# Kernel tuning notes

Measured on AMD Instinct MI355X. Metric: run time of the kernel, lower is better.

## Reference

```python
import jax, jax.numpy as jnp
import numpy as np

H = 64  # LSTM units for both layers
T = 128  # sequence length
D = 128  # input feature dim
B = 2048  # batch

def setup_inputs() -> dict:
    key = jax.random.key(0)
    ks = jax.random.split(key, 7)
    s_in = 1.0 / np.sqrt(D)
    s_h = 1.0 / np.sqrt(H)
    return {
        "x": jax.random.normal(ks[0], (B, T, D), dtype=jnp.float32),
        # Keras LSTM weights: kernel [in, 4H], recurrent_kernel [H, 4H], bias [4H]
        # gate order: i, f, g (cell candidate), o
        "W1": jax.random.normal(ks[1], (D, 4 * H), dtype=jnp.float32) * s_in,
        "U1": jax.random.normal(ks[2], (H, 4 * H), dtype=jnp.float32) * s_h,
        "b1": jnp.zeros((4 * H,), dtype=jnp.float32),
        "W2": jax.random.normal(ks[3], (H, 4 * H), dtype=jnp.float32) * s_h,
        "U2": jax.random.normal(ks[4], (H, 4 * H), dtype=jnp.float32) * s_h,
        "b2": jnp.zeros((4 * H,), dtype=jnp.float32),
    }

def _lstm(x, W, U, b, act):
    """Keras-faithful LSTM, return_sequences=True, zero init state.
    x: [B, T, D_in] -> hs: [B, T, H]
    recurrent_activation = sigmoid; `act` is the cell/output activation.
    """
    Bsz = x.shape[0]
    # Precompute input projections for all timesteps (one big GEMM).
    xz = jnp.einsum('btd,dg->btg', x, W) + b  # [B, T, 4H]
    xz = jnp.swapaxes(xz, 0, 1)  # [T, B, 4H]

    def step(carry, zt):
        h, c = carry
        z = zt + h @ U  # [B, 4H]
        i, f, g, o = jnp.split(z, 4, axis=-1)
        i = jax.nn.sigmoid(i)
        f = jax.nn.sigmoid(f)
        g = act(g)
        o = jax.nn.sigmoid(o)
        c = f * c + i * g
        h = o * act(c)
        return (h, c), h

    init = (jnp.zeros((Bsz, H), x.dtype), jnp.zeros((Bsz, H), x.dtype))
    _, hs = jax.lax.scan(step, init, xz)  # hs: [T, B, H]
    return jnp.swapaxes(hs, 0, 1)  # [B, T, H]

def reference(x, W1, U1, b1, W2, U2, b2):
    h1 = _lstm(x, W1, U1, b1, jnp.tanh)           # layer 1: default tanh
    h2 = _lstm(h1, W2, U2, b2, jax.nn.sigmoid)    # layer 2: activation='sigmoid'
    return h2.reshape(h2.shape[0], T * H, 1)      # Reshape((8192, 1))
```

## Files before the change

### kernel.cpp

```cpp
#include <hip/hip_runtime.h>
#include <stdint.h>

typedef __attribute__((ext_vector_type(8))) short short8;
typedef __attribute__((ext_vector_type(4))) short short4_t;
typedef __attribute__((ext_vector_type(4))) float floatx4;

#define TT 128
#define DD 128

#define BARRIER_LDS() asm volatile("s_waitcnt lgkmcnt(0)\n\ts_barrier" ::: "memory")

__device__ __forceinline__ short f2bf(float f) {
  union { float f; uint32_t u; } v; v.f = f;
  uint32_t u = v.u;
  u += 0x7fffu + ((u >> 16) & 1u);
  return (short)(u >> 16);
}

__device__ __forceinline__ float sigf(float x) {
  return __builtin_amdgcn_rcpf(1.f + __expf(-x));
}
__device__ __forceinline__ float tanhf_(float x) {
  return 2.f * __builtin_amdgcn_rcpf(1.f + __expf(-2.f * x)) - 1.f;
}

__global__ void wtrans_all(const float* __restrict__ W1, const float* __restrict__ U1,
                           const float* __restrict__ W2, const float* __restrict__ U2,
                           short* __restrict__ w1t, short* __restrict__ u1t,
                           short* __restrict__ w2t, short* __restrict__ u2t) {
  int n = blockIdx.x;
  int k = threadIdx.x;
  w1t[n * 128 + k] = f2bf(W1[k * 256 + n]);
  if (k < 64) {
    u1t[n * 64 + k] = f2bf(U1[k * 256 + n]);
    w2t[n * 64 + k] = f2bf(W2[k * 256 + n]);
    u2t[n * 64 + k] = f2bf(U2[k * 256 + n]);
  }
}

__global__ __launch_bounds__(512, 2) void lstm_fused(
    const float* __restrict__ x,
    const short* __restrict__ w1t, const short* __restrict__ u1t,
    const short* __restrict__ w2t, const short* __restrict__ u2t,
    const float* __restrict__ b1, const float* __restrict__ b2,
    float* __restrict__ out) {
  __shared__ short hb1[2][8 * 80];
  __shared__ short hb2[2][8 * 80];
  __shared__ short xbuf[2][8 * 144];

  const int tid = threadIdx.x;
  const int w = tid >> 6;
  const bool isL1 = (w < 4);
  const int wg = w & 3;
  const int lane = tid & 63;
  const int mrow = lane & 15;
  const int quad = lane >> 4;
  const int rowbase = blockIdx.x * 8;
  const int colw = wg * 16 + mrow;
  const int br_a = 2 * (mrow >> 2) + (mrow & 1);

  short8 wA[4][4], uA[4][2];
  float bias[4];
  if (isL1) {
#pragma unroll
    for (int g = 0; g < 4; ++g) {
      const int n = g * 4 + wg;
#pragma unroll
      for (int s = 0; s < 4; ++s)
        wA[g][s] = *(const short8*)(w1t + n * 2048 + mrow * 128 + quad * 8 + s * 32);
#pragma unroll
      for (int s = 0; s < 2; ++s)
        uA[g][s] = *(const short8*)(u1t + n * 1024 + mrow * 64 + quad * 8 + s * 32);
      bias[g] = b1[g * 64 + colw];
    }
  } else {
#pragma unroll
    for (int g = 0; g < 4; ++g) {
      const int n = g * 4 + wg;
#pragma unroll
      for (int s = 0; s < 2; ++s) {
        wA[g][s]     = *(const short8*)(w2t + n * 1024 + mrow * 64 + quad * 8 + s * 32);
        wA[g][2 + s] = *(const short8*)(u2t + n * 1024 + mrow * 64 + quad * 8 + s * 32);
      }
      bias[g] = b2[g * 64 + colw];
    }
  }

  const int tid2 = tid & 255;
  const int sxr = tid2 >> 5;
  const int sxc = (tid2 & 31) * 4;
  const float* xload = x + (size_t)(rowbase + sxr) * (TT * DD) + sxc;

  short8 h1f[2], xh[4];
#pragma unroll
  for (int s = 0; s < 2; ++s)
#pragma unroll
    for (int j = 0; j < 8; ++j) h1f[s][j] = 0;
#pragma unroll
  for (int s = 0; s < 4; ++s)
#pragma unroll
    for (int j = 0; j < 8; ++j) xh[s][j] = 0;
  float cc[2] = {0.f, 0.f};
  floatx4 xnext;

  for (int idx = tid; idx < 2 * 8 * 80; idx += 512) ((short*)hb2)[idx] = 0;
  if (!isL1) {
    floatx4 x0 = *(const floatx4*)xload;
    short4_t v;
#pragma unroll
    for (int j = 0; j < 4; ++j) v[j] = f2bf(x0[j]);
    *(short4_t*)&xbuf[0][sxr * 144 + sxc] = v;
    xnext = *(const floatx4*)(xload + DD);
  }
  BARRIER_LDS();
  if (isL1) {
#pragma unroll
    for (int s = 0; s < 4; ++s)
      xh[s] = *(const short8*)&xbuf[0][br_a * 144 + (quad + 4 * s) * 8];
  }

  float* outp = out + (size_t)rowbase * 8192 + colw;

#pragma unroll 1
  for (int i = 0; i <= TT; ++i) {
    const int p = i & 1;

    if (isL1) {
      if (i < TT) {
        floatx4 acc[4];
#pragma unroll
        for (int g = 0; g < 4; ++g) acc[g] = floatx4{0.f, 0.f, 0.f, 0.f};
#pragma unroll
        for (int g = 0; g < 4; ++g) {
#pragma unroll
          for (int s = 0; s < 4; ++s)
            acc[g] = __builtin_amdgcn_mfma_f32_16x16x32_bf16(xh[s], wA[g][s], acc[g], 0, 0, 0);
#pragma unroll
          for (int s = 0; s < 2; ++s)
            acc[g] = __builtin_amdgcn_mfma_f32_16x16x32_bf16(h1f[s], uA[g][s], acc[g], 0, 0, 0);
        }
#pragma unroll
        for (int r = 0; r < 2; ++r) {
          float ig = sigf(acc[0][r] + bias[0]);
          float fg = sigf(acc[1][r] + bias[1]);
          float gg = tanhf_(acc[2][r] + bias[2]);
          float og = sigf(acc[3][r] + bias[3]);
          float c = fg * cc[r] + ig * gg;
          cc[r] = c;
          float h = og * tanhf_(c);
          hb1[p][(2 * quad + r) * 80 + colw] = f2bf(h);
        }
      }
    } else {
      {
        short4_t v;
#pragma unroll
        for (int j = 0; j < 4; ++j) v[j] = f2bf(xnext[j]);
        *(short4_t*)&xbuf[1 - p][sxr * 144 + sxc] = v;
        int tn = (i + 2 < TT) ? i + 2 : TT - 1;
        xnext = *(const floatx4*)(xload + (size_t)tn * DD);
      }
      if (i >= 1) {
        floatx4 acc[4];
#pragma unroll
        for (int g = 0; g < 4; ++g) acc[g] = floatx4{0.f, 0.f, 0.f, 0.f};
#pragma unroll
        for (int g = 0; g < 4; ++g) {
#pragma unroll
          for (int s = 0; s < 2; ++s)
            acc[g] = __builtin_amdgcn_mfma_f32_16x16x32_bf16(h1f[s], wA[g][s], acc[g], 0, 0, 0);
#pragma unroll
          for (int s = 0; s < 2; ++s)
            acc[g] = __builtin_amdgcn_mfma_f32_16x16x32_bf16(xh[s], wA[g][2 + s], acc[g], 0, 0, 0);
        }
#pragma unroll
        for (int r = 0; r < 2; ++r) {
          float ig = sigf(acc[0][r] + bias[0]);
          float fg = sigf(acc[1][r] + bias[1]);
          float gg = sigf(acc[2][r] + bias[2]);
          float og = sigf(acc[3][r] + bias[3]);
          float c = fg * cc[r] + ig * gg;
          cc[r] = c;
          float h = og * sigf(c);
          hb2[p][(2 * quad + r) * 80 + colw] = f2bf(h);
          outp[(size_t)(2 * quad + r) * 8192 + (i - 1) * 64] = h;
        }
      }
    }

    BARRIER_LDS();

    if (i < TT) {
      if (isL1) {
#pragma unroll
        for (int s = 0; s < 2; ++s)
          h1f[s] = *(const short8*)&hb1[p][br_a * 80 + (quad + 4 * s) * 8];
#pragma unroll
        for (int s = 0; s < 4; ++s)
          xh[s] = *(const short8*)&xbuf[1 - p][br_a * 144 + (quad + 4 * s) * 8];
      } else {
#pragma unroll
        for (int s = 0; s < 2; ++s) {
          h1f[s] = *(const short8*)&hb1[p][br_a * 80 + (quad + 4 * s) * 8];
          xh[s]  = *(const short8*)&hb2[p][br_a * 80 + (quad + 4 * s) * 8];
        }
      }
    }
  }
}

extern "C" void kernel_launch(void* const* d_in, const int* in_sizes, int n_in,
                              void* d_out, int out_size, void* d_ws, size_t ws_size,
                              hipStream_t stream) {
  const float* x  = (const float*)d_in[0];
  const float* W1 = (const float*)d_in[1];
  const float* U1 = (const float*)d_in[2];
  const float* b1 = (const float*)d_in[3];
  const float* W2 = (const float*)d_in[4];
  const float* U2 = (const float*)d_in[5];
  const float* b2 = (const float*)d_in[6];
  float* out = (float*)d_out;

  short* w1t = (short*)d_ws;
  short* u1t = w1t + 32768;
  short* w2t = u1t + 16384;
  short* u2t = w2t + 16384;

  hipLaunchKernelGGL(wtrans_all, dim3(256), dim3(128), 0, stream,
                     W1, U1, W2, U2, w1t, u1t, w2t, u2t);
  hipLaunchKernelGGL(lstm_fused, dim3(256), dim3(512), 0, stream,
                     x, w1t, u1t, w2t, u2t, b1, b2, out);
}
```

Measured before the change: 287.4 us.

## Split LSTM into four wave-group stages pipelining input and recurrent projections

The block grows from 512 to 1024 threads, organised as four 4-wave jobs. Job 0 computes the x·W1 projection, job 1 does the U1 recurrence, job 2 computes h1·W2 and job 3 does the U2 recurrence and writes the output. Partial gate sums pass between jobs through new double-buffered fp32 LDS arrays, skewed by one timestep per stage. This takes the non-recurrent GEMM work off the serial critical path of each layer, at the cost of more LDS, more barrier participants per step, three extra pipeline steps, and launch bounds of (1024,4) that may force tight register limits.

```diff
diff --git a/kernel.cpp b/kernel.cpp
--- a/kernel.cpp
+++ b/kernel.cpp
@@ -4,6 +4,7 @@
 typedef __attribute__((ext_vector_type(8))) short short8;
 typedef __attribute__((ext_vector_type(4))) short short4_t;
 typedef __attribute__((ext_vector_type(4))) float floatx4;
+typedef __attribute__((ext_vector_type(2))) float floatx2;
 
 #define TT 128
 #define DD 128
@@ -38,7 +39,7 @@
   }
 }
 
-__global__ __launch_bounds__(512, 2) void lstm_fused(
+__global__ __launch_bounds__(1024, 4) void lstm_fused(
     const float* __restrict__ x,
     const short* __restrict__ w1t, const short* __restrict__ u1t,
     const short* __restrict__ w2t, const short* __restrict__ u2t,
@@ -47,10 +48,12 @@
   __shared__ short hb1[2][8 * 80];
   __shared__ short hb2[2][8 * 80];
   __shared__ short xbuf[2][8 * 144];
+  __shared__ float zx[2][256][10];
+  __shared__ float zw2[2][256][10];
 
   const int tid = threadIdx.x;
   const int w = tid >> 6;
-  const bool isL1 = (w < 4);
+  const int job = w >> 2;
   const int wg = w & 3;
   const int lane = tid & 63;
   const int mrow = lane & 15;
@@ -59,85 +62,94 @@
   const int colw = wg * 16 + mrow;
   const int br_a = 2 * (mrow >> 2) + (mrow & 1);
 
-  short8 wA[4][4], uA[4][2];
-  float bias[4];
-  if (isL1) {
-#pragma unroll
-    for (int g = 0; g < 4; ++g) {
-      const int n = g * 4 + wg;
-#pragma unroll
-      for (int s = 0; s < 4; ++s)
-        wA[g][s] = *(const short8*)(w1t + n * 2048 + mrow * 128 + quad * 8 + s * 32);
-#pragma unroll
-      for (int s = 0; s < 2; ++s)
-        uA[g][s] = *(const short8*)(u1t + n * 1024 + mrow * 64 + quad * 8 + s * 32);
-      bias[g] = b1[g * 64 + colw];
-    }
-  } else {
-#pragma unroll
-    for (int g = 0; g < 4; ++g) {
-      const int n = g * 4 + wg;
-#pragma unroll
-      for (int s = 0; s < 2; ++s) {
-        wA[g][s]     = *(const short8*)(w2t + n * 1024 + mrow * 64 + quad * 8 + s * 32);
-        wA[g][2 + s] = *(const short8*)(u2t + n * 1024 + mrow * 64 + quad * 8 + s * 32);
-      }
-      bias[g] = b2[g * 64 + colw];
-    }
+  for (int idx = tid; idx < 2 * 8 * 80; idx += 1024) {
+    ((short*)hb1)[idx] = 0;
+    ((short*)hb2)[idx] = 0;
   }
 
   const int tid2 = tid & 255;
   const int sxr = tid2 >> 5;
   const int sxc = (tid2 & 31) * 4;
   const float* xload = x + (size_t)(rowbase + sxr) * (TT * DD) + sxc;
-
-  short8 h1f[2], xh[4];
-#pragma unroll
-  for (int s = 0; s < 2; ++s)
-#pragma unroll
-    for (int j = 0; j < 8; ++j) h1f[s][j] = 0;
-#pragma unroll
-  for (int s = 0; s < 4; ++s)
-#pragma unroll
-    for (int j = 0; j < 8; ++j) xh[s][j] = 0;
-  float cc[2] = {0.f, 0.f};
-  floatx4 xnext;
-
-  for (int idx = tid; idx < 2 * 8 * 80; idx += 512) ((short*)hb2)[idx] = 0;
-  if (!isL1) {
+  floatx4 xcur, xnxt;
+  if (job == 0) {
     floatx4 x0 = *(const floatx4*)xload;
     short4_t v;
 #pragma unroll
     for (int j = 0; j < 4; ++j) v[j] = f2bf(x0[j]);
     *(short4_t*)&xbuf[0][sxr * 144 + sxc] = v;
-    xnext = *(const floatx4*)(xload + DD);
-  }
+    xcur = *(const floatx4*)(xload + DD);
+    xnxt = *(const floatx4*)(xload + 2 * DD);
+  }
+
   BARRIER_LDS();
-  if (isL1) {
-#pragma unroll
-    for (int s = 0; s < 4; ++s)
-      xh[s] = *(const short8*)&xbuf[0][br_a * 144 + (quad + 4 * s) * 8];
-  }
-
-  float* outp = out + (size_t)rowbase * 8192 + colw;
-
-#pragma unroll 1
-  for (int i = 0; i <= TT; ++i) {
-    const int p = i & 1;
-
-    if (isL1) {
+
+  if (job == 0) {
+    short8 wA[4][4];
+#pragma unroll
+    for (int g = 0; g < 4; ++g) {
+      const int n = g * 4 + wg;
+#pragma unroll
+      for (int s = 0; s < 4; ++s)
+        wA[g][s] = *(const short8*)(w1t + n * 2048 + mrow * 128 + quad * 8 + s * 32);
+    }
+#pragma unroll 1
+    for (int i = 0; i <= TT + 2; ++i) {
+      const int p = i & 1;
       if (i < TT) {
         floatx4 acc[4];
 #pragma unroll
         for (int g = 0; g < 4; ++g) acc[g] = floatx4{0.f, 0.f, 0.f, 0.f};
 #pragma unroll
+        for (int s = 0; s < 4; ++s) {
+          short8 xh = *(const short8*)&xbuf[p][br_a * 144 + (quad + 4 * s) * 8];
+#pragma unroll
+          for (int g = 0; g < 4; ++g)
+            acc[g] = __builtin_amdgcn_mfma_f32_16x16x32_bf16(xh, wA[g][s], acc[g], 0, 0, 0);
+        }
+        if (i <= TT - 2) {
+          short4_t v;
+#pragma unroll
+          for (int j = 0; j < 4; ++j) v[j] = f2bf(xcur[j]);
+          *(short4_t*)&xbuf[1 - p][sxr * 144 + sxc] = v;
+          xcur = xnxt;
+          const int tn = (i + 3 < TT) ? (i + 3) : (TT - 1);
+          xnxt = *(const floatx4*)(xload + (size_t)tn * DD);
+        }
+#pragma unroll
+        for (int g = 0; g < 4; ++g)
+          *(floatx2*)&zx[p][g * 64 + colw][2 * quad] = floatx2{acc[g][0], acc[g][1]};
+      }
+      BARRIER_LDS();
+    }
+  } else if (job == 1) {
+    short8 uA[4][2];
+    float bias[4];
+#pragma unroll
+    for (int g = 0; g < 4; ++g) {
+      const int n = g * 4 + wg;
+#pragma unroll
+      for (int s = 0; s < 2; ++s)
+        uA[g][s] = *(const short8*)(u1t + n * 1024 + mrow * 64 + quad * 8 + s * 32);
+      bias[g] = b1[g * 64 + colw];
+    }
+    float cc[2] = {0.f, 0.f};
+#pragma unroll 1
+    for (int i = 0; i <= TT + 2; ++i) {
+      const int p = i & 1;
+      if (i >= 1 && i <= TT) {
+        floatx4 acc[4];
+#pragma unroll
         for (int g = 0; g < 4; ++g) {
-#pragma unroll
-          for (int s = 0; s < 4; ++s)
-            acc[g] = __builtin_amdgcn_mfma_f32_16x16x32_bf16(xh[s], wA[g][s], acc[g], 0, 0, 0);
-#pragma unroll
-          for (int s = 0; s < 2; ++s)
-            acc[g] = __builtin_amdgcn_mfma_f32_16x16x32_bf16(h1f[s], uA[g][s], acc[g], 0, 0, 0);
+          floatx2 z = *(const floatx2*)&zx[1 - p][g * 64 + colw][2 * quad];
+          acc[g] = floatx4{z[0], z[1], z[0], z[1]};
+        }
+#pragma unroll
+        for (int s = 0; s < 2; ++s) {
+          short8 hf = *(const short8*)&hb1[p][br_a * 80 + (quad + 4 * s) * 8];
+#pragma unroll
+          for (int g = 0; g < 4; ++g)
+            acc[g] = __builtin_amdgcn_mfma_f32_16x16x32_bf16(hf, uA[g][s], acc[g], 0, 0, 0);
         }
 #pragma unroll
         for (int r = 0; r < 2; ++r) {
@@ -148,30 +160,70 @@
           float c = fg * cc[r] + ig * gg;
           cc[r] = c;
           float h = og * tanhf_(c);
-          hb1[p][(2 * quad + r) * 80 + colw] = f2bf(h);
-        }
-      }
-    } else {
-      {
-        short4_t v;
-#pragma unroll
-        for (int j = 0; j < 4; ++j) v[j] = f2bf(xnext[j]);
-        *(short4_t*)&xbuf[1 - p][sxr * 144 + sxc] = v;
-        int tn = (i + 2 < TT) ? i + 2 : TT - 1;
-        xnext = *(const floatx4*)(xload + (size_t)tn * DD);
-      }
-      if (i >= 1) {
+          hb1[1 - p][(2 * quad + r) * 80 + colw] = f2bf(h);
+        }
+      }
+      BARRIER_LDS();
+    }
+  } else if (job == 2) {
+    short8 wB[4][2];
+#pragma unroll
+    for (int g = 0; g < 4; ++g) {
+      const int n = g * 4 + wg;
+#pragma unroll
+      for (int s = 0; s < 2; ++s)
+        wB[g][s] = *(const short8*)(w2t + n * 1024 + mrow * 64 + quad * 8 + s * 32);
+    }
+#pragma unroll 1
+    for (int i = 0; i <= TT + 2; ++i) {
+      const int p = i & 1;
+      if (i >= 2 && i <= TT + 1) {
         floatx4 acc[4];
 #pragma unroll
         for (int g = 0; g < 4; ++g) acc[g] = floatx4{0.f, 0.f, 0.f, 0.f};
 #pragma unroll
+        for (int s = 0; s < 2; ++s) {
+          short8 hf = *(const short8*)&hb1[p][br_a * 80 + (quad + 4 * s) * 8];
+#pragma unroll
+          for (int g = 0; g < 4; ++g)
+            acc[g] = __builtin_amdgcn_mfma_f32_16x16x32_bf16(hf, wB[g][s], acc[g], 0, 0, 0);
+        }
+#pragma unroll
+        for (int g = 0; g < 4; ++g)
+          *(floatx2*)&zw2[p][g * 64 + colw][2 * quad] = floatx2{acc[g][0], acc[g][1]};
+      }
+      BARRIER_LDS();
+    }
+  } else {
+    short8 uB[4][2];
+    float bias[4];
+#pragma unroll
+    for (int g = 0; g < 4; ++g) {
+      const int n = g * 4 + wg;
+#pragma unroll
+      for (int s = 0; s < 2; ++s)
+        uB[g][s] = *(const short8*)(u2t + n * 1024 + mrow * 64 + quad * 8 + s * 32);
+      bias[g] = b2[g * 64 + colw];
+    }
+    float cc[2] = {0.f, 0.f};
+    float* outp = out + (size_t)rowbase * 8192 + colw;
+#pragma unroll 1
+    for (int i = 0; i <= TT + 2; ++i) {
+      const int p = i & 1;
+      if (i >= 3) {
+        const int t = i - 3;
+        floatx4 acc[4];
+#pragma unroll
         for (int g = 0; g < 4; ++g) {
-#pragma unroll
-          for (int s = 0; s < 2; ++s)
-            acc[g] = __builtin_amdgcn_mfma_f32_16x16x32_bf16(h1f[s], wA[g][s], acc[g], 0, 0, 0);
-#pragma unroll
-          for (int s = 0; s < 2; ++s)
-            acc[g] = __builtin_amdgcn_mfma_f32_16x16x32_bf16(xh[s], wA[g][2 + s], acc[g], 0, 0, 0);
+          floatx2 z = *(const floatx2*)&zw2[1 - p][g * 64 + colw][2 * quad];
+          acc[g] = floatx4{z[0], z[1], z[0], z[1]};
+        }
+#pragma unroll
+        for (int s = 0; s < 2; ++s) {
+          short8 hf = *(const short8*)&hb2[p][br_a * 80 + (quad + 4 * s) * 8];
+#pragma unroll
+          for (int g = 0; g < 4; ++g)
+            acc[g] = __builtin_amdgcn_mfma_f32_16x16x32_bf16(hf, uB[g][s], acc[g], 0, 0, 0);
         }
 #pragma unroll
         for (int r = 0; r < 2; ++r) {
@@ -182,29 +234,11 @@
           float c = fg * cc[r] + ig * gg;
           cc[r] = c;
           float h = og * sigf(c);
-          hb2[p][(2 * quad + r) * 80 + colw] = f2bf(h);
-          outp[(size_t)(2 * quad + r) * 8192 + (i - 1) * 64] = h;
-        }
-      }
-    }
-
-    BARRIER_LDS();
-
-    if (i < TT) {
-      if (isL1) {
-#pragma unroll
-        for (int s = 0; s < 2; ++s)
-          h1f[s] = *(const short8*)&hb1[p][br_a * 80 + (quad + 4 * s) * 8];
-#pragma unroll
-        for (int s = 0; s < 4; ++s)
-          xh[s] = *(const short8*)&xbuf[1 - p][br_a * 144 + (quad + 4 * s) * 8];
-      } else {
-#pragma unroll
-        for (int s = 0; s < 2; ++s) {
-          h1f[s] = *(const short8*)&hb1[p][br_a * 80 + (quad + 4 * s) * 8];
-          xh[s]  = *(const short8*)&hb2[p][br_a * 80 + (quad + 4 * s) * 8];
-        }
-      }
+          hb2[1 - p][(2 * quad + r) * 80 + colw] = f2bf(h);
+          outp[(size_t)(2 * quad + r) * 8192 + t * 64] = h;
+        }
+      }
+      BARRIER_LDS();
     }
   }
 }
@@ -228,6 +262,6 @@
 
   hipLaunchKernelGGL(wtrans_all, dim3(256), dim3(128), 0, stream,
                      W1, U1, W2, U2, w1t, u1t, w2t, u2t);
-  hipLaunchKernelGGL(lstm_fused, dim3(256), dim3(512), 0, stream,
+  hipLaunchKernelGGL(lstm_fused, dim3(256), dim3(1024), 0, stream,
                      x, w1t, u1t, w2t, u2t, b1, b2, out);
 }
```

Measured after the change: 310.2 us. 7.9% more time.

## Halve batch rows per block to double grid size and raise occupancy

Applied to the files above, without the earlier changes.

Each block now handles 4 batch rows instead of 8, and the grid grows to 512 blocks. In the MFMA tiles the rows are duplicated, so each lane evaluates the gate nonlinearities for a single row instead of two. Launch bounds are raised to 4 blocks per CU, and the x prefetch goes two steps ahead. The aim is to spread the latency-bound sequential recurrence across more CUs and more resident waves, shortening the per-step critical path. The cost is that half of the MFMA work is redundant, and register pressure under the tighter launch bounds could cause spills.

```diff
diff --git a/kernel.cpp b/kernel.cpp
--- a/kernel.cpp
+++ b/kernel.cpp
@@ -2,8 +2,9 @@
 #include <stdint.h>
 
 typedef __attribute__((ext_vector_type(8))) short short8;
-typedef __attribute__((ext_vector_type(4))) short short4_t;
+typedef __attribute__((ext_vector_type(2))) short short2_t;
 typedef __attribute__((ext_vector_type(4))) float floatx4;
+typedef __attribute__((ext_vector_type(2))) float floatx2;
 
 #define TT 128
 #define DD 128
@@ -38,15 +39,15 @@
   }
 }
 
-__global__ __launch_bounds__(512, 2) void lstm_fused(
+__global__ __launch_bounds__(512, 4) void lstm_fused(
     const float* __restrict__ x,
     const short* __restrict__ w1t, const short* __restrict__ u1t,
     const short* __restrict__ w2t, const short* __restrict__ u2t,
     const float* __restrict__ b1, const float* __restrict__ b2,
     float* __restrict__ out) {
-  __shared__ short hb1[2][8 * 80];
-  __shared__ short hb2[2][8 * 80];
-  __shared__ short xbuf[2][8 * 144];
+  __shared__ short hb1[2][4 * 80];
+  __shared__ short hb2[2][4 * 80];
+  __shared__ short xbuf[2][4 * 144];
 
   const int tid = threadIdx.x;
   const int w = tid >> 6;
@@ -55,9 +56,11 @@
   const int lane = tid & 63;
   const int mrow = lane & 15;
   const int quad = lane >> 4;
-  const int rowbase = blockIdx.x * 8;
+  const int rowbase = blockIdx.x * 4;
   const int colw = wg * 16 + mrow;
-  const int br_a = 2 * (mrow >> 2) + (mrow & 1);
+  const int br_a = (2 * (mrow >> 2) + (mrow & 1)) & 3;
+  const bool rsel = (quad >> 1) & 1;
+  const int erow = (2 * quad + (quad >> 1)) & 3;
 
   short8 wA[4][4], uA[4][2];
   float bias[4];
@@ -87,8 +90,8 @@
   }
 
   const int tid2 = tid & 255;
-  const int sxr = tid2 >> 5;
-  const int sxc = (tid2 & 31) * 4;
+  const int sxr = tid2 >> 6;
+  const int sxc = (tid2 & 63) * 2;
   const float* xload = x + (size_t)(rowbase + sxr) * (TT * DD) + sxc;
 
   short8 h1f[2], xh[4];
@@ -100,17 +103,17 @@
   for (int s = 0; s < 4; ++s)
 #pragma unroll
     for (int j = 0; j < 8; ++j) xh[s][j] = 0;
-  float cc[2] = {0.f, 0.f};
-  floatx4 xnext;
-
-  for (int idx = tid; idx < 2 * 8 * 80; idx += 512) ((short*)hb2)[idx] = 0;
+  float cc = 0.f;
+  floatx2 xcur, xnxt;
+
+  for (int idx = tid; idx < 2 * 4 * 80; idx += 512) ((short*)hb2)[idx] = 0;
   if (!isL1) {
-    floatx4 x0 = *(const floatx4*)xload;
-    short4_t v;
-#pragma unroll
-    for (int j = 0; j < 4; ++j) v[j] = f2bf(x0[j]);
-    *(short4_t*)&xbuf[0][sxr * 144 + sxc] = v;
-    xnext = *(const floatx4*)(xload + DD);
+    floatx2 x0 = *(const floatx2*)xload;
+    short2_t v;
+    v[0] = f2bf(x0[0]); v[1] = f2bf(x0[1]);
+    *(short2_t*)&xbuf[0][sxr * 144 + sxc] = v;
+    xcur = *(const floatx2*)(xload + DD);
+    xnxt = *(const floatx2*)(xload + 2 * DD);
   }
   BARRIER_LDS();
   if (isL1) {
@@ -139,26 +142,28 @@
           for (int s = 0; s < 2; ++s)
             acc[g] = __builtin_amdgcn_mfma_f32_16x16x32_bf16(h1f[s], uA[g][s], acc[g], 0, 0, 0);
         }
-#pragma unroll
-        for (int r = 0; r < 2; ++r) {
-          float ig = sigf(acc[0][r] + bias[0]);
-          float fg = sigf(acc[1][r] + bias[1]);
-          float gg = tanhf_(acc[2][r] + bias[2]);
-          float og = sigf(acc[3][r] + bias[3]);
-          float c = fg * cc[r] + ig * gg;
-          cc[r] = c;
+        float za[4];
+#pragma unroll
+        for (int g = 0; g < 4; ++g) za[g] = rsel ? acc[g][1] : acc[g][0];
+        {
+          float ig = sigf(za[0] + bias[0]);
+          float fg = sigf(za[1] + bias[1]);
+          float gg = tanhf_(za[2] + bias[2]);
+          float og = sigf(za[3] + bias[3]);
+          float c = fg * cc + ig * gg;
+          cc = c;
           float h = og * tanhf_(c);
-          hb1[p][(2 * quad + r) * 80 + colw] = f2bf(h);
+          hb1[p][erow * 80 + colw] = f2bf(h);
         }
       }
     } else {
-      {
-        short4_t v;
-#pragma unroll
-        for (int j = 0; j < 4; ++j) v[j] = f2bf(xnext[j]);
-        *(short4_t*)&xbuf[1 - p][sxr * 144 + sxc] = v;
-        int tn = (i + 2 < TT) ? i + 2 : TT - 1;
-        xnext = *(const floatx4*)(xload + (size_t)tn * DD);
+      if (i <= TT - 2) {
+        short2_t v;
+        v[0] = f2bf(xcur[0]); v[1] = f2bf(xcur[1]);
+        *(short2_t*)&xbuf[1 - p][sxr * 144 + sxc] = v;
+        xcur = xnxt;
+        const int tn = (i + 3 < TT) ? (i + 3) : (TT - 1);
+        xnxt = *(const floatx2*)(xload + (size_t)tn * DD);
       }
       if (i >= 1) {
         floatx4 acc[4];
@@ -173,17 +178,19 @@
           for (int s = 0; s < 2; ++s)
             acc[g] = __builtin_amdgcn_mfma_f32_16x16x32_bf16(xh[s], wA[g][2 + s], acc[g], 0, 0, 0);
         }
-#pragma unroll
-        for (int r = 0; r < 2; ++r) {
-          float ig = sigf(acc[0][r] + bias[0]);
-          float fg = sigf(acc[1][r] + bias[1]);
-          float gg = sigf(acc[2][r] + bias[2]);
-          float og = sigf(acc[3][r] + bias[3]);
-          float c = fg * cc[r] + ig * gg;
-          cc[r] = c;
+        float za[4];
+#pragma unroll
+        for (int g = 0; g < 4; ++g) za[g] = rsel ? acc[g][1] : acc[g][0];
+        {
+          float ig = sigf(za[0] + bias[0]);
+          float fg = sigf(za[1] + bias[1]);
+          float gg = sigf(za[2] + bias[2]);
+          float og = sigf(za[3] + bias[3]);
+          float c = fg * cc + ig * gg;
+          cc = c;
           float h = og * sigf(c);
-          hb2[p][(2 * quad + r) * 80 + colw] = f2bf(h);
-          outp[(size_t)(2 * quad + r) * 8192 + (i - 1) * 64] = h;
+          hb2[p][erow * 80 + colw] = f2bf(h);
+          outp[(size_t)erow * 8192 + (i - 1) * 64] = h;
         }
       }
     }
@@ -228,6 +235,6 @@
 
   hipLaunchKernelGGL(wtrans_all, dim3(256), dim3(128), 0, stream,
                      W1, U1, W2, U2, w1t, u1t, w2t, u2t);
-  hipLaunchKernelGGL(lstm_fused, dim3(256), dim3(512), 0, stream,
+  hipLaunchKernelGGL(lstm_fused, dim3(512), dim3(512), 0, stream,
                      x, w1t, u1t, w2t, u2t, b1, b2, out);
 }
```

After: 531.0 us. +84.8%, slower.

## Split LSTM step into two barrier phases so layers alternate MFMA and activation

Applied to the files above, without the earlier changes.

Each timestep now has two half-phases separated by barriers. In one half the layer-1 waves run MFMAs while the layer-2 waves do their gate activations, and in the other half the roles swap. This lets the matrix and vector units overlap across the two wave groups instead of each wave serialising MFMA then transcendental work. Double-buffered LDS is replaced with single buffers, the x prefetch goes one step deeper, and the MFMA loops are reordered to interleave gates. The cost is two barriers per step instead of one and a two-step skew for layer 2.

```diff
diff --git a/kernel.cpp b/kernel.cpp
--- a/kernel.cpp
+++ b/kernel.cpp
@@ -9,6 +9,7 @@
 #define DD 128
 
 #define BARRIER_LDS() asm volatile("s_waitcnt lgkmcnt(0)\n\ts_barrier" ::: "memory")
+#define SCHED_FENCE() __builtin_amdgcn_sched_barrier(0)
 
 __device__ __forceinline__ short f2bf(float f) {
   union { float f; uint32_t u; } v; v.f = f;
@@ -44,9 +45,9 @@
     const short* __restrict__ w2t, const short* __restrict__ u2t,
     const float* __restrict__ b1, const float* __restrict__ b2,
     float* __restrict__ out) {
-  __shared__ short hb1[2][8 * 80];
-  __shared__ short hb2[2][8 * 80];
-  __shared__ short xbuf[2][8 * 144];
+  __shared__ short hb1[8 * 80];
+  __shared__ short hb2[8 * 80];
+  __shared__ short xbuf[8 * 144];
 
   const int tid = threadIdx.x;
   const int w = tid >> 6;
@@ -92,53 +93,86 @@
   const float* xload = x + (size_t)(rowbase + sxr) * (TT * DD) + sxc;
 
   short8 h1f[2], xh[4];
-#pragma unroll
-  for (int s = 0; s < 2; ++s)
-#pragma unroll
-    for (int j = 0; j < 8; ++j) h1f[s][j] = 0;
-#pragma unroll
-  for (int s = 0; s < 4; ++s)
-#pragma unroll
-    for (int j = 0; j < 8; ++j) xh[s][j] = 0;
+  floatx4 acc[4];
   float cc[2] = {0.f, 0.f};
-  floatx4 xnext;
-
-  for (int idx = tid; idx < 2 * 8 * 80; idx += 512) ((short*)hb2)[idx] = 0;
+  floatx4 xcur, xnxt;
+
+  for (int idx = tid; idx < 8 * 80; idx += 512) { hb1[idx] = 0; hb2[idx] = 0; }
   if (!isL1) {
     floatx4 x0 = *(const floatx4*)xload;
     short4_t v;
 #pragma unroll
     for (int j = 0; j < 4; ++j) v[j] = f2bf(x0[j]);
-    *(short4_t*)&xbuf[0][sxr * 144 + sxc] = v;
-    xnext = *(const floatx4*)(xload + DD);
+    *(short4_t*)&xbuf[sxr * 144 + sxc] = v;
+    xcur = *(const floatx4*)(xload + DD);
+    xnxt = *(const floatx4*)(xload + 2 * DD);
   }
   BARRIER_LDS();
   if (isL1) {
 #pragma unroll
     for (int s = 0; s < 4; ++s)
-      xh[s] = *(const short8*)&xbuf[0][br_a * 144 + (quad + 4 * s) * 8];
-  }
+      xh[s] = *(const short8*)&xbuf[br_a * 144 + (quad + 4 * s) * 8];
+  }
+  BARRIER_LDS();
 
   float* outp = out + (size_t)rowbase * 8192 + colw;
 
 #pragma unroll 1
-  for (int i = 0; i <= TT; ++i) {
-    const int p = i & 1;
-
+  for (int i = 0; i <= TT + 1; ++i) {
     if (isL1) {
       if (i < TT) {
-        floatx4 acc[4];
+        h1f[0] = *(const short8*)&hb1[br_a * 80 + quad * 8];
+        h1f[1] = *(const short8*)&hb1[br_a * 80 + (quad + 4) * 8];
 #pragma unroll
         for (int g = 0; g < 4; ++g) acc[g] = floatx4{0.f, 0.f, 0.f, 0.f};
 #pragma unroll
-        for (int g = 0; g < 4; ++g) {
-#pragma unroll
-          for (int s = 0; s < 4; ++s)
+        for (int s = 0; s < 4; ++s)
+#pragma unroll
+          for (int g = 0; g < 4; ++g)
             acc[g] = __builtin_amdgcn_mfma_f32_16x16x32_bf16(xh[s], wA[g][s], acc[g], 0, 0, 0);
 #pragma unroll
-          for (int s = 0; s < 2; ++s)
+        for (int s = 0; s < 2; ++s)
+#pragma unroll
+          for (int g = 0; g < 4; ++g)
             acc[g] = __builtin_amdgcn_mfma_f32_16x16x32_bf16(h1f[s], uA[g][s], acc[g], 0, 0, 0);
+      }
+    } else {
+      if (i <= TT - 2) {
+        short4_t v;
+#pragma unroll
+        for (int j = 0; j < 4; ++j) v[j] = f2bf(xcur[j]);
+        *(short4_t*)&xbuf[sxr * 144 + sxc] = v;
+        xcur = xnxt;
+        const int tn = (i + 3 < TT) ? (i + 3) : (TT - 1);
+        xnxt = *(const floatx4*)(xload + (size_t)tn * DD);
+      }
+      if (i >= 1 && i <= TT) {
+        h1f[0] = *(const short8*)&hb1[br_a * 80 + quad * 8];
+        h1f[1] = *(const short8*)&hb1[br_a * 80 + (quad + 4) * 8];
+      }
+      if (i >= 2) {
+        const int t = i - 2;
+#pragma unroll
+        for (int r = 0; r < 2; ++r) {
+          float ig = sigf(acc[0][r] + bias[0]);
+          float fg = sigf(acc[1][r] + bias[1]);
+          float gg = sigf(acc[2][r] + bias[2]);
+          float og = sigf(acc[3][r] + bias[3]);
+          float c = fg * cc[r] + ig * gg;
+          cc[r] = c;
+          float h = og * sigf(c);
+          hb2[(2 * quad + r) * 80 + colw] = f2bf(h);
+          outp[(size_t)(2 * quad + r) * 8192 + t * 64] = h;
         }
+      }
+    }
+
+    SCHED_FENCE();
+    BARRIER_LDS();
+    SCHED_FENCE();
+
+    if (isL1) {
+      if (i < TT) {
 #pragma unroll
         for (int r = 0; r < 2; ++r) {
           float ig = sigf(acc[0][r] + bias[0]);
@@ -148,64 +182,36 @@
           float c = fg * cc[r] + ig * gg;
           cc[r] = c;
           float h = og * tanhf_(c);
-          hb1[p][(2 * quad + r) * 80 + colw] = f2bf(h);
+          hb1[(2 * quad + r) * 80 + colw] = f2bf(h);
         }
       }
+      if (i <= TT - 2) {
+#pragma unroll
+        for (int s = 0; s < 4; ++s)
+          xh[s] = *(const short8*)&xbuf[br_a * 144 + (quad + 4 * s) * 8];
+      }
     } else {
-      {
-        short4_t v;
-#pragma unroll
-        for (int j = 0; j < 4; ++j) v[j] = f2bf(xnext[j]);
-        *(short4_t*)&xbuf[1 - p][sxr * 144 + sxc] = v;
-        int tn = (i + 2 < TT) ? i + 2 : TT - 1;
-        xnext = *(const floatx4*)(xload + (size_t)tn * DD);
-      }
-      if (i >= 1) {
-        floatx4 acc[4];
+      if (i >= 1 && i <= TT) {
+        xh[0] = *(const short8*)&hb2[br_a * 80 + quad * 8];
+        xh[1] = *(const short8*)&hb2[br_a * 80 + (quad + 4) * 8];
 #pragma unroll
         for (int g = 0; g < 4; ++g) acc[g] = floatx4{0.f, 0.f, 0.f, 0.f};
 #pragma unroll
-        for (int g = 0; g < 4; ++g) {
-#pragma unroll
-          for (int s = 0; s < 2; ++s)
+        for (int s = 0; s < 2; ++s)
+#pragma unroll
+          for (int g = 0; g < 4; ++g)
             acc[g] = __builtin_amdgcn_mfma_f32_16x16x32_bf16(h1f[s], wA[g][s], acc[g], 0, 0, 0);
 #pragma unroll
-          for (int s = 0; s < 2; ++s)
+        for (int s = 0; s < 2; ++s)
+#pragma unroll
+          for (int g = 0; g < 4; ++g)
             acc[g] = __builtin_amdgcn_mfma_f32_16x16x32_bf16(xh[s], wA[g][2 + s], acc[g], 0, 0, 0);
-        }
-#pragma unroll
-        for (int r = 0; r < 2; ++r) {
-          float ig = sigf(acc[0][r] + bias[0]);
-          float fg = sigf(acc[1][r] + bias[1]);
-          float gg = sigf(acc[2][r] + bias[2]);
-          float og = sigf(acc[3][r] + bias[3]);
-          float c = fg * cc[r] + ig * gg;
-          cc[r] = c;
-          float h = og * sigf(c);
-          hb2[p][(2 * quad + r) * 80 + colw] = f2bf(h);
-          outp[(size_t)(2 * quad + r) * 8192 + (i - 1) * 64] = h;
-        }
-      }
-    }
-
+      }
+    }
+
+    SCHED_FENCE();
     BARRIER_LDS();
-
-    if (i < TT) {
-      if (isL1) {
-#pragma unroll
-        for (int s = 0; s < 2; ++s)
-          h1f[s] = *(const short8*)&hb1[p][br_a * 80 + (quad + 4 * s) * 8];
-#pragma unroll
-        for (int s = 0; s < 4; ++s)
-          xh[s] = *(const short8*)&xbuf[1 - p][br_a * 144 + (quad + 4 * s) * 8];
-      } else {
-#pragma unroll
-        for (int s = 0; s < 2; ++s) {
-          h1f[s] = *(const short8*)&hb1[p][br_a * 80 + (quad + 4 * s) * 8];
-          xh[s]  = *(const short8*)&hb2[p][br_a * 80 + (quad + 4 * s) * 8];
-        }
-      }
-    }
+    SCHED_FENCE();
   }
 }
 
```

New measurement: 304.7 us. +6.0%, slower.
